# Optimization experiments

Measured on AMD Instinct MI355X. Metric: run time of the kernel, lower is better.

The kernel has to match this reference:

```python
import jax, jax.numpy as jnp
import numpy as np

B, N, NP, NS = 8, 4096, 1024, 32
CF = 64            # input point-feature channels; in_channel = 3 + CF = 67
MLP = [64, 128, 256]
EPS = 1e-5         # BatchNorm eps (torch default)


def setup_inputs() -> dict:
    key = jax.random.key(0)
    ks = jax.random.split(key, 8)
    inp = {
        "xyz": jax.random.normal(ks[0], (B, N, 3), jnp.float32),
        "points": jax.random.normal(ks[1], (B, CF, N), jnp.float32),
        "sample_idx": jax.random.randint(ks[2], (B, NP), 0, N, dtype=jnp.int32),
        "neighbor_idx": jax.random.randint(ks[3], (B, NP, NS), 0, N, dtype=jnp.int32),
    }
    c = 3 + CF
    for i, o in enumerate(MLP):
        wk = jax.random.fold_in(ks[4], i)
        inp[f"W{i}"] = jax.random.normal(wk, (o, c), jnp.float32) * (1.0 / np.sqrt(c))
        inp[f"b{i}"] = jnp.zeros((o,), jnp.float32)
        inp[f"gamma{i}"] = jnp.ones((o,), jnp.float32)
        inp[f"beta{i}"] = jnp.zeros((o,), jnp.float32)
        c = o
    return inp


def _forward(xyz, points, sample_idx, neighbor_idx, params):
    # xyz: (B,N,3)  points: (B,CF,N)
    new_xyz = jnp.take_along_axis(xyz, sample_idx[:, :, None], axis=1)        # (B,NP,3)
    nbr_xyz = jax.vmap(lambda x, idx: x[idx])(xyz, neighbor_idx)               # (B,NP,NS,3)
    rel = nbr_xyz - new_xyz[:, :, None, :]                                     # (B,NP,NS,3)
    nbr_feat = jax.vmap(lambda f, idx: f[:, idx])(points, neighbor_idx)        # (B,CF,NP,NS)
    x = jnp.concatenate([rel.transpose(0, 3, 1, 2), nbr_feat], axis=1)         # (B,3+CF,NP,NS)
    # 1x1 Conv2d -> BatchNorm2d (training-mode batch stats) -> ReLU stack
    for W, b, g, be in params:
        x = jnp.einsum('oc,bcps->bops', W, x) + b[None, :, None, None]
        mu = x.mean(axis=(0, 2, 3), keepdims=True)
        var = x.var(axis=(0, 2, 3), keepdims=True)
        x = g[None, :, None, None] * (x - mu) * jax.lax.rsqrt(var + EPS) + be[None, :, None, None]
        x = jax.nn.relu(x)
    new_points = x.max(axis=-1)                                                # (B,C_out,NP)
    return new_xyz, new_points


def reference(xyz, points, sample_idx, neighbor_idx,
              W0, b0, gamma0, beta0,
              W1, b1, gamma1, beta1,
              W2, b2, gamma2, beta2):
    params = [(W0, b0, gamma0, beta0), (W1, b1, gamma1, beta1), (W2, b2, gamma2, beta2)]
    return _forward(xyz, points, sample_idx, neighbor_idx, params)
```

## Files before the change

### kernel.cpp

```cpp
#include <hip/hip_runtime.h>

typedef unsigned short u16;
typedef unsigned int u32;
typedef __attribute__((ext_vector_type(8))) short short8;
typedef __attribute__((ext_vector_type(16))) float f32x16;

#define BB 8
#define NN 4096
#define NPP 1024
#define NSS 32
#define CFF 64
#define C0 67
#define H0 64
#define H1 128
#define H2 256
#define NTOT (BB*NN)
#define MTOT (BB*NPP*NSS)
#define BN_EPS 1e-5f
#define INV_M (1.0f/262144.0f)
#define NSLOT 64
#define SQOFF 16384
#define LSTRIDE 32768

#define MFMA32(a,b,c) __builtin_amdgcn_mfma_f32_32x32x16_bf16(a,b,c,0,0,0)

__device__ __forceinline__ float bf2f(u16 h){ return __uint_as_float(((u32)h)<<16); }
__device__ __forceinline__ u16 f2bf(float f){
  u32 u = __float_as_uint(f);
  u32 r = (u + 0x7fffu + ((u>>16)&1u)) >> 16;
  return (u16)r;
}
__device__ __forceinline__ u32 pack2(float a, float b){
  return (u32)f2bf(a) | ((u32)f2bf(b)<<16);
}

#define WS_NEED 42434560u

__global__ __launch_bounds__(256) void k_setup(
    const float* __restrict__ xyz, const int* __restrict__ sidx,
    const float* __restrict__ W0, const float* __restrict__ W1, const float* __restrict__ W2,
    u16* __restrict__ Wt0c, u16* __restrict__ Wt1c, u16* __restrict__ Wt2c,
    float* __restrict__ out_newxyz)
{
  int blk = blockIdx.x, tid = threadIdx.x;
  if (blk < 32) {
    int t0 = blk*256 + tid;
    int b = t0 >> 10;
    int s = sidx[t0];
    for (int k = 0; k < 3; ++k)
      out_newxyz[(size_t)t0*3 + k] = xyz[((size_t)(b*NN + s))*3 + k];
  } else if (blk == 32) {
    for (int i = 0; i < 20; ++i) {
      int e = i*256 + tid;
      if (e >= 5120) break;
      int kc = e >> 9, o = (e >> 3) & 63, j = e & 7;
      float v;
      if (kc < 8)       v = W0[o*C0 + 3 + kc*8 + j];
      else if (kc == 8) v = (j < 3) ? W0[o*C0 + j] : 0.f;
      else              v = 0.f;
      Wt0c[e] = f2bf(v);
    }
  } else if (blk == 33) {
    for (int i = 0; i < 32; ++i) {
      int e = i*256 + tid;
      int kc = e >> 10, n = (e >> 3) & 127, j = e & 7;
      Wt1c[e] = f2bf(W1[n*H0 + kc*8 + j]);
    }
  } else {
    int base = (blk - 34) * 4096;
    for (int i = 0; i < 16; ++i) {
      int e = base + i*256 + tid;
      int kc = e >> 11, n = (e >> 3) & 255, j = e & 7;
      Wt2c[e] = f2bf(W2[n*H1 + kc*8 + j]);
    }
  }
}

__global__ __launch_bounds__(256) void k_xyz_only(
    const float* __restrict__ xyz, const int* __restrict__ sidx, float* __restrict__ out_newxyz)
{
  int t0 = blockIdx.x*256 + threadIdx.x;
  int b = t0 >> 10;
  int s = sidx[t0];
  for (int k = 0; k < 3; ++k)
    out_newxyz[(size_t)t0*3 + k] = xyz[((size_t)(b*NN + s))*3 + k];
}

__global__ __launch_bounds__(256) void k_fin(
    const float* __restrict__ stIn, const float* __restrict__ gma,
    const float* __restrict__ bta, int nch,
    float* __restrict__ sclG, float* __restrict__ sftG)
{
  int c = threadIdx.x;
  if (c < nch) {
    float s = 0.f, q = 0.f;
    for (int sl = 0; sl < NSLOT; ++sl) { s += stIn[sl*256 + c]; q += stIn[SQOFF + sl*256 + c]; }
    float mu = s*INV_M, var = q*INV_M - mu*mu;
    float sc = gma[c] * rsqrtf(var + BN_EPS);
    sclG[c] = sc; sftG[c] = bta[c] - mu*sc;
  }
}

__global__ __launch_bounds__(256) void k_uv(
    const float* __restrict__ xyz, const float* __restrict__ points,
    const u16* __restrict__ Wt0c, u16* __restrict__ U, u16* __restrict__ T)
{
  __shared__ u16 XLc[10*128*8];
  __shared__ u16 W0c[10*64*8];
  int tid = threadIdx.x;
  int gn0 = blockIdx.x * 128;
  int b = gn0 >> 12;
  int n0 = gn0 & 4095;

  for (int i = 0; i < 3; ++i) {
    int e = i*256 + tid;
    if (e < 640) ((uint4*)W0c)[e] = ((const uint4*)Wt0c)[e];
  }
  {
    int c = tid >> 2, nseg = tid & 3;
    const float* src = points + ((size_t)(b*CFF + c))*NN + n0 + nseg*32;
    int cb = c >> 3, cr = c & 7;
    for (int t = 0; t < 8; ++t) {
      float4 v = *(const float4*)(src + t*4);
      int n = nseg*32 + t*4;
      XLc[(cb*128 + n+0)*8 + cr] = f2bf(v.x);
      XLc[(cb*128 + n+1)*8 + cr] = f2bf(v.y);
      XLc[(cb*128 + n+2)*8 + cr] = f2bf(v.z);
      XLc[(cb*128 + n+3)*8 + cr] = f2bf(v.w);
    }
  }
  if (tid < 128) {
    int gn = gn0 + tid;
    float x = xyz[(size_t)gn*3+0], y = xyz[(size_t)gn*3+1], z = xyz[(size_t)gn*3+2];
    uint4 v = { pack2(x,y), pack2(z,0.f), 0u, 0u };
    *(uint4*)&XLc[(8*128 + tid)*8] = v;
  } else {
    uint4 z4 = {0u,0u,0u,0u};
    *(uint4*)&XLc[(9*128 + (tid-128))*8] = z4;
  }
  __syncthreads();

  int lane = tid & 63, wv = tid >> 6, l31 = lane & 31, kh = lane >> 5;
  int nt = wv & 1, mtb = (wv >> 1)*2;
  f32x16 accT2[2], accU2[2];
  for (int mi = 0; mi < 2; ++mi) for (int r = 0; r < 16; ++r) accT2[mi][r] = 0.f;

  {
    int ck = 8 + kh;
    short8 bfrag = *(const short8*)&W0c[(ck*64 + nt*32 + l31)*8];
    for (int mi = 0; mi < 2; ++mi) {
      short8 afrag = *(const short8*)&XLc[(ck*128 + (mtb+mi)*32 + l31)*8];
      accT2[mi] = MFMA32(afrag, bfrag, accT2[mi]);
    }
  }
  for (int mi = 0; mi < 2; ++mi) accU2[mi] = accT2[mi];
  for (int kt = 0; kt < 4; ++kt) {
    int ck = kt*2 + kh;
    short8 bfrag = *(const short8*)&W0c[(ck*64 + nt*32 + l31)*8];
    for (int mi = 0; mi < 2; ++mi) {
      short8 afrag = *(const short8*)&XLc[(ck*128 + (mtb+mi)*32 + l31)*8];
      accU2[mi] = MFMA32(afrag, bfrag, accU2[mi]);
    }
  }

  int c = nt*32 + l31;
  for (int mi = 0; mi < 2; ++mi)
    for (int r = 0; r < 16; ++r) {
      int gm = gn0 + (mtb+mi)*32 + (r&3) + 8*(r>>2) + 4*kh;
      U[(size_t)gm*64 + c] = f2bf(accU2[mi][r]);
      T[(size_t)gm*64 + c] = f2bf(accT2[mi][r]);
    }
}

__global__ __launch_bounds__(256) void k_s0y(
    const int* __restrict__ sidx, const int* __restrict__ nidx,
    const u16* __restrict__ U, const u16* __restrict__ T,
    u16* __restrict__ y0, float* __restrict__ stats)
{
  int tid = threadIdx.x;
  int m0 = blockIdx.x * 128;
  int b = m0 >> 15;
  int c0 = (tid & 7) * 8;
  int rg = tid >> 3;
  int wv = tid >> 6;
  int mbase = m0 + rg*4;
  int p = (mbase & 32767) >> 5;
  int sp = sidx[b*NPP + p];
  u16 tv[8];
  *(uint4*)tv = *(const uint4*)(T + ((size_t)(b*NN + sp))*64 + c0);
  float tf[8], s[8], q[8];
  for (int j = 0; j < 8; ++j) { tf[j] = bf2f(tv[j]); s[j] = 0.f; q[j] = 0.f; }
  int nb[4];
  for (int i = 0; i < 4; ++i) nb[i] = nidx[mbase + i];
  for (int i = 0; i < 4; ++i) {
    u16 uv[8], ov[8];
    *(uint4*)uv = *(const uint4*)(U + ((size_t)(b*NN + nb[i]))*64 + c0);
    for (int j = 0; j < 8; ++j) {
      float d = bf2f(uv[j]) - tf[j];
      s[j] += d; q[j] += d*d;
      ov[j] = f2bf(d);
    }
    *(uint4*)(y0 + ((size_t)(mbase + i))*64 + c0) = *(uint4*)ov;
  }
  for (int msk = 8; msk <= 32; msk <<= 1)
    for (int j = 0; j < 8; ++j) {
      s[j] += __shfl_xor(s[j], msk);
      q[j] += __shfl_xor(q[j], msk);
    }
  if ((tid & 63) < 8) {
    int slot = (blockIdx.x*4 + wv) & 63;
    for (int j = 0; j < 8; ++j) {
      atomicAdd(&stats[slot*256 + c0 + j], s[j]);
      atomicAdd(&stats[SQOFF + slot*256 + c0 + j], q[j]);
    }
  }
}

__global__ __launch_bounds__(256) void k_l1s(
    const u16* __restrict__ y0, const u16* __restrict__ Wt1c,
    const float* __restrict__ sclG0, const float* __restrict__ sftG0,
    float* __restrict__ stOut)
{
  __shared__ u16 X0c[8*128*8];
  __shared__ u16 W1c[8*128*8];
  __shared__ float scl0[64], sft0[64];
  int tid = threadIdx.x;
  int m0 = blockIdx.x * 128;

  if (tid < 64) { scl0[tid] = sclG0[tid]; sft0[tid] = sftG0[tid]; }
  for (int i = 0; i < 4; ++i)
    ((uint4*)W1c)[i*256 + tid] = ((const uint4*)Wt1c)[i*256 + tid];

  int pos = tid & 127, half = tid >> 7;
  {
    const u16* row = y0 + (size_t)(m0 + pos)*64 + half*32;
    u16 hs[32];
    for (int t = 0; t < 4; ++t) *(uint4*)&hs[t*8] = ((const uint4*)row)[t];
    __syncthreads();
    u16 ob[32];
    for (int j = 0; j < 32; ++j) {
      int c = half*32 + j;
      ob[j] = f2bf(fmaxf(fmaf(scl0[c], bf2f(hs[j]), sft0[c]), 0.f));
    }
    for (int t = 0; t < 4; ++t)
      *(uint4*)&X0c[((half*4+t)*128 + pos)*8] = *(uint4*)&ob[t*8];
  }
  __syncthreads();

  int lane = tid & 63, wv = tid >> 6, l31 = lane & 31, kh = lane >> 5;
  f32x16 acc[4];
  for (int mt = 0; mt < 4; ++mt) for (int r = 0; r < 16; ++r) acc[mt][r] = 0.f;

  for (int kt = 0; kt < 4; ++kt) {
    int ck = kt*2 + kh;
    short8 bfrag = *(const short8*)&W1c[(ck*128 + wv*32 + l31)*8];
    for (int mt = 0; mt < 4; ++mt) {
      short8 afrag = *(const short8*)&X0c[(ck*128 + mt*32 + l31)*8];
      acc[mt] = MFMA32(afrag, bfrag, acc[mt]);
    }
  }

  float s = 0.f, q = 0.f;
  for (int mt = 0; mt < 4; ++mt)
    for (int r = 0; r < 16; ++r) { float y = acc[mt][r]; s += y; q += y*y; }
  s += __shfl_xor(s, 32); q += __shfl_xor(q, 32);
  if (lane < 32) {
    int slot = (blockIdx.x*4 + wv) & 63;
    atomicAdd(&stOut[slot*256 + wv*32 + lane], s);
    atomicAdd(&stOut[SQOFF + slot*256 + wv*32 + lane], q);
  }
}

__global__ __launch_bounds__(256) void k_l2f(
    const u16* __restrict__ y0,
    const u16* __restrict__ Wt1c, const u16* __restrict__ Wt2c,
    const float* __restrict__ sclG0, const float* __restrict__ sftG0,
    const float* __restrict__ sclG1, const float* __restrict__ sftG1,
    float* __restrict__ stOut, u16* __restrict__ mxp, u16* __restrict__ mnp)
{
  __shared__ u16 X1c[16*520];
  __shared__ u16 UB[16384];
  __shared__ float scl0[64], sft0[64], scl1[128], sft1[128];
  int tid = threadIdx.x;
  int m0 = blockIdx.x * 64;

  if (tid < 64) { scl0[tid] = sclG0[tid]; sft0[tid] = sftG0[tid]; }
  if (tid < 128) { scl1[tid] = sclG1[tid]; sft1[tid] = sftG1[tid]; }
  u16* X0c = UB;
  u16* W1c = UB + 4096;
  for (int i = 0; i < 4; ++i)
    ((uint4*)W1c)[i*256 + tid] = ((const uint4*)Wt1c)[i*256 + tid];

  int pos = tid & 63, grp = tid >> 6;
  {
    const u16* row = y0 + (size_t)(m0 + pos)*64 + grp*16;
    u16 hs[16];
    *(uint4*)&hs[0] = ((const uint4*)row)[0];
    *(uint4*)&hs[8] = ((const uint4*)row)[1];
    __syncthreads();
    u16 ob[16];
    for (int j = 0; j < 16; ++j) {
      int c = grp*16 + j;
      ob[j] = f2bf(fmaxf(fmaf(scl0[c], bf2f(hs[j]), sft0[c]), 0.f));
    }
    *(uint4*)&X0c[((2*grp)*64 + pos)*8]   = *(uint4*)&ob[0];
    *(uint4*)&X0c[((2*grp+1)*64 + pos)*8] = *(uint4*)&ob[8];
  }
  __syncthreads();

  int lane = tid & 63, wv = tid >> 6, l31 = lane & 31, kh = lane >> 5;

  f32x16 acc1[2];
  for (int nt = 0; nt < 2; ++nt) for (int r = 0; r < 16; ++r) acc1[nt][r] = 0.f;
  for (int kt = 0; kt < 4; ++kt) {
    int ck = kt*2 + kh;
    short8 afrag = *(const short8*)&W1c[(ck*128 + wv*32 + l31)*8];
    for (int nt = 0; nt < 2; ++nt) {
      short8 bfrag = *(const short8*)&X0c[(ck*64 + nt*32 + l31)*8];
      acc1[nt] = MFMA32(afrag, bfrag, acc1[nt]);
    }
  }
  __syncthreads();

  {
    float s1r[16], f1r[16];
    for (int r = 0; r < 16; ++r) {
      int ch = wv*32 + (r&3) + 8*(r>>2) + 4*kh;
      s1r[r] = scl1[ch]; f1r[r] = sft1[ch];
    }
    for (int nt = 0; nt < 2; ++nt) {
      int posn = nt*32 + l31;
      for (int g = 0; g < 4; ++g) {
        float v0 = fmaxf(fmaf(s1r[g*4+0], acc1[nt][g*4+0], f1r[g*4+0]), 0.f);
        float v1 = fmaxf(fmaf(s1r[g*4+1], acc1[nt][g*4+1], f1r[g*4+1]), 0.f);
        float v2 = fmaxf(fmaf(s1r[g*4+2], acc1[nt][g*4+2], f1r[g*4+2]), 0.f);
        float v3 = fmaxf(fmaf(s1r[g*4+3], acc1[nt][g*4+3], f1r[g*4+3]), 0.f);
        uint2 w = { pack2(v0, v1), pack2(v2, v3) };
        *(uint2*)&X1c[(wv*4 + g)*520 + posn*8 + 4*kh] = w;
      }
    }
  }
  __syncthreads();

  f32x16 acc2[2][2];
  for (int nt = 0; nt < 2; ++nt) for (int mt = 0; mt < 2; ++mt)
    for (int r = 0; r < 16; ++r) acc2[nt][mt][r] = 0.f;

  for (int h = 0; h < 2; ++h) {
    for (int i = 0; i < 8; ++i)
      ((uint4*)UB)[i*256 + tid] = ((const uint4*)Wt2c)[h*2048 + i*256 + tid];
    __syncthreads();
    for (int k4 = 0; k4 < 4; ++k4) {
      int ckx = (h*4 + k4)*2 + kh;
      int ckw = k4*2 + kh;
      short8 a[2], bf_[2];
      for (int mt = 0; mt < 2; ++mt) a[mt]  = *(const short8*)&X1c[ckx*520 + (mt*32 + l31)*8];
      for (int nt = 0; nt < 2; ++nt) bf_[nt] = *(const short8*)&UB[(ckw*256 + wv*64 + nt*32 + l31)*8];
      for (int nt = 0; nt < 2; ++nt)
        for (int mt = 0; mt < 2; ++mt)
          acc2[nt][mt] = MFMA32(a[mt], bf_[nt], acc2[nt][mt]);
    }
    __syncthreads();
  }

  int slot = (blockIdx.x*4 + wv) & 63;
  for (int nt = 0; nt < 2; ++nt) {
    float s = 0.f, q = 0.f;
    float mx[2] = {-3.0e38f, -3.0e38f}, mn[2] = {3.0e38f, 3.0e38f};
    for (int mt = 0; mt < 2; ++mt)
      for (int r = 0; r < 16; ++r) {
        float y = acc2[nt][mt][r];
        s += y; q += y*y;
        mx[mt] = fmaxf(mx[mt], y); mn[mt] = fminf(mn[mt], y);
      }
    s += __shfl_xor(s, 32); q += __shfl_xor(q, 32);
    mx[0] = fmaxf(mx[0], __shfl_xor(mx[0], 32));
    mx[1] = fmaxf(mx[1], __shfl_xor(mx[1], 32));
    mn[0] = fminf(mn[0], __shfl_xor(mn[0], 32));
    mn[1] = fminf(mn[1], __shfl_xor(mn[1], 32));
    if (lane < 32) {
      int c = wv*64 + nt*32 + lane;
      atomicAdd(&stOut[slot*256 + c], s);
      atomicAdd(&stOut[SQOFF + slot*256 + c], q);
      for (int mt = 0; mt < 2; ++mt) {
        size_t pr = (size_t)blockIdx.x*2 + mt;
        mxp[pr*H2 + c] = f2bf(mx[mt]);
        mnp[pr*H2 + c] = f2bf(mn[mt]);
      }
    }
  }
}

__global__ __launch_bounds__(256) void k_final(
    const u16* __restrict__ mxp, const u16* __restrict__ mnp,
    const float* __restrict__ sclG2, const float* __restrict__ sftG2,
    float* __restrict__ out_np)
{
  __shared__ float tmp[256][33];
  int tid = threadIdx.x;
  int b = blockIdx.x >> 5;
  int p0 = (blockIdx.x & 31) * 32;

  float sc = sclG2[tid];
  float sh = sftG2[tid];

  for (int pp = 0; pp < 32; ++pp) {
    size_t base = ((size_t)(b*NPP + p0 + pp))*H2 + tid;
    float xv = bf2f(mxp[base]), nv = bf2f(mnp[base]);
    float v = (sc >= 0.f) ? fmaf(sc, xv, sh) : fmaf(sc, nv, sh);
    tmp[tid][pp] = fmaxf(v, 0.f);
  }
  __syncthreads();

  int pl = tid & 31, cg = tid >> 5;
  for (int cc = 0; cc < 32; ++cc) {
    int c = cc*8 + cg;
    out_np[((size_t)b*H2 + c)*NPP + p0 + pl] = tmp[c][pl];
  }
}

extern "C" void kernel_launch(void* const* d_in, const int* in_sizes, int n_in,
                              void* d_out, int out_size, void* d_ws, size_t ws_size,
                              hipStream_t stream)
{
  const float* xyz    = (const float*)d_in[0];
  const float* points = (const float*)d_in[1];
  const int*   sidx   = (const int*)d_in[2];
  const int*   nidx   = (const int*)d_in[3];
  const float* W0 = (const float*)d_in[4];
  const float* g0 = (const float*)d_in[6];
  const float* e0 = (const float*)d_in[7];
  const float* W1 = (const float*)d_in[8];
  const float* g1 = (const float*)d_in[10];
  const float* e1 = (const float*)d_in[11];
  const float* W2 = (const float*)d_in[12];
  const float* g2 = (const float*)d_in[14];
  const float* e2 = (const float*)d_in[15];

  float* out_xyz = (float*)d_out;
  float* out_np  = out_xyz + (size_t)BB*NPP*3;

  if (ws_size < (size_t)WS_NEED) {
    hipMemsetAsync(out_np, 0, (size_t)BB*H2*NPP*4, stream);
    k_xyz_only<<<32, 256, 0, stream>>>(xyz, sidx, out_xyz);
    return;
  }

  char* ws = (char*)d_ws;
  float* stats = (float*)(ws + 0);
  u16*   Wt0c  = (u16*)(ws + 393216);
  u16*   Wt1c  = (u16*)(ws + 403456);
  u16*   Wt2c  = (u16*)(ws + 419840);
  float* bnc   = (float*)(ws + 485376);
  u16*   Ubuf  = (u16*)(ws + 491520);
  u16*   Tbuf  = (u16*)(ws + 4685824);
  u16*   y0    = (u16*)(ws + 8880128);
  u16*   mxp   = Ubuf;
  u16*   mnp   = Tbuf;
  float *scl0G = bnc,        *sft0G = bnc + 256;
  float *scl1G = bnc + 512,  *sft1G = bnc + 768;
  float *scl2G = bnc + 1024, *sft2G = bnc + 1280;

  hipMemsetAsync(stats, 0, 3*LSTRIDE*sizeof(float), stream);
  k_setup<<<42, 256, 0, stream>>>(xyz, sidx, W0, W1, W2, Wt0c, Wt1c, Wt2c, out_xyz);
  k_uv<<<NTOT/128, 256, 0, stream>>>(xyz, points, Wt0c, Ubuf, Tbuf);
  k_s0y<<<MTOT/128, 256, 0, stream>>>(sidx, nidx, Ubuf, Tbuf, y0, stats);
  k_fin<<<1, 256, 0, stream>>>(stats, g0, e0, 64, scl0G, sft0G);
  k_l1s<<<MTOT/128, 256, 0, stream>>>(y0, Wt1c, scl0G, sft0G, stats + LSTRIDE);
  k_fin<<<1, 256, 0, stream>>>(stats + LSTRIDE, g1, e1, 128, scl1G, sft1G);
  k_l2f<<<MTOT/64, 256, 0, stream>>>(y0, Wt1c, Wt2c,
                                     scl0G, sft0G, scl1G, sft1G,
                                     stats + 2*LSTRIDE, mxp, mnp);
  k_fin<<<1, 256, 0, stream>>>(stats + 2*LSTRIDE, g2, e2, 256, scl2G, sft2G);
  k_final<<<256, 256, 0, stream>>>(mxp, mnp, scl2G, sft2G, out_np);
}
```

Before: 207.6 us.

## Fold BN finalize into producer kernels via last-block counters and merge setup into k_uv

Removes the three single-block k_fin launches. Each statistics-producing kernel now bumps a global counter, and the last block to finish reduces the slot partials into scale and shift. The weight-prep kernel is merged into the U/T projection kernel, and each projection block converts W0 into shared memory itself. The W2 staging buffer in k_l2f is shrunk and loaded in four smaller chunks, which trades lower LDS use (possibly higher occupancy) for more barriers. Together these cut launch count and inter-kernel gaps, at the cost of a serialized tail reduction in the last block.

```diff
diff --git a/kernel.cpp b/kernel.cpp
--- a/kernel.cpp
+++ b/kernel.cpp
@@ -34,87 +34,66 @@
   return (u32)f2bf(a) | ((u32)f2bf(b)<<16);
 }
 
-#define WS_NEED 42434560u
-
-__global__ __launch_bounds__(256) void k_setup(
-    const float* __restrict__ xyz, const int* __restrict__ sidx,
+#define WS_NEED 42424576u
+
+__global__ __launch_bounds__(256) void k_xyz_only(
+    const float* __restrict__ xyz, const int* __restrict__ sidx, float* __restrict__ out_newxyz)
+{
+  int t0 = blockIdx.x*256 + threadIdx.x;
+  int b = t0 >> 10;
+  int s = sidx[t0];
+  for (int k = 0; k < 3; ++k)
+    out_newxyz[(size_t)t0*3 + k] = xyz[((size_t)(b*NN + s))*3 + k];
+}
+
+__global__ __launch_bounds__(256) void k_init(
+    const float* __restrict__ xyz, const float* __restrict__ points,
+    const int* __restrict__ sidx,
     const float* __restrict__ W0, const float* __restrict__ W1, const float* __restrict__ W2,
-    u16* __restrict__ Wt0c, u16* __restrict__ Wt1c, u16* __restrict__ Wt2c,
-    float* __restrict__ out_newxyz)
+    u16* __restrict__ Wt1c, u16* __restrict__ Wt2c,
+    u16* __restrict__ U, u16* __restrict__ T, float* __restrict__ out_newxyz)
 {
   int blk = blockIdx.x, tid = threadIdx.x;
-  if (blk < 32) {
-    int t0 = blk*256 + tid;
-    int b = t0 >> 10;
-    int s = sidx[t0];
-    for (int k = 0; k < 3; ++k)
-      out_newxyz[(size_t)t0*3 + k] = xyz[((size_t)(b*NN + s))*3 + k];
-  } else if (blk == 32) {
-    for (int i = 0; i < 20; ++i) {
-      int e = i*256 + tid;
-      if (e >= 5120) break;
+  if (blk >= 256) {
+    if (blk < 288) {
+      int t0 = (blk - 256)*256 + tid;
+      int b = t0 >> 10;
+      int s = sidx[t0];
+      for (int k = 0; k < 3; ++k)
+        out_newxyz[(size_t)t0*3 + k] = xyz[((size_t)(b*NN + s))*3 + k];
+    } else if (blk == 288) {
+      for (int i = 0; i < 32; ++i) {
+        int e = i*256 + tid;
+        int kc = e >> 10, n = (e >> 3) & 127, j = e & 7;
+        Wt1c[e] = f2bf(W1[n*H0 + kc*8 + j]);
+      }
+    } else {
+      int base = (blk - 289) * 4096;
+      for (int i = 0; i < 16; ++i) {
+        int e = base + i*256 + tid;
+        int kc = e >> 11, n = (e >> 3) & 255, j = e & 7;
+        Wt2c[e] = f2bf(W2[n*H1 + kc*8 + j]);
+      }
+    }
+    return;
+  }
+
+  __shared__ u16 XLc[10*128*8];
+  __shared__ u16 W0c[10*64*8];
+  int gn0 = blk * 128;
+  int b = gn0 >> 12;
+  int n0 = gn0 & 4095;
+
+  for (int i = 0; i < 20; ++i) {
+    int e = i*256 + tid;
+    if (e < 5120) {
       int kc = e >> 9, o = (e >> 3) & 63, j = e & 7;
       float v;
       if (kc < 8)       v = W0[o*C0 + 3 + kc*8 + j];
       else if (kc == 8) v = (j < 3) ? W0[o*C0 + j] : 0.f;
       else              v = 0.f;
-      Wt0c[e] = f2bf(v);
-    }
-  } else if (blk == 33) {
-    for (int i = 0; i < 32; ++i) {
-      int e = i*256 + tid;
-      int kc = e >> 10, n = (e >> 3) & 127, j = e & 7;
-      Wt1c[e] = f2bf(W1[n*H0 + kc*8 + j]);
-    }
-  } else {
-    int base = (blk - 34) * 4096;
-    for (int i = 0; i < 16; ++i) {
-      int e = base + i*256 + tid;
-      int kc = e >> 11, n = (e >> 3) & 255, j = e & 7;
-      Wt2c[e] = f2bf(W2[n*H1 + kc*8 + j]);
-    }
-  }
-}
-
-__global__ __launch_bounds__(256) void k_xyz_only(
-    const float* __restrict__ xyz, const int* __restrict__ sidx, float* __restrict__ out_newxyz)
-{
-  int t0 = blockIdx.x*256 + threadIdx.x;
-  int b = t0 >> 10;
-  int s = sidx[t0];
-  for (int k = 0; k < 3; ++k)
-    out_newxyz[(size_t)t0*3 + k] = xyz[((size_t)(b*NN + s))*3 + k];
-}
-
-__global__ __launch_bounds__(256) void k_fin(
-    const float* __restrict__ stIn, const float* __restrict__ gma,
-    const float* __restrict__ bta, int nch,
-    float* __restrict__ sclG, float* __restrict__ sftG)
-{
-  int c = threadIdx.x;
-  if (c < nch) {
-    float s = 0.f, q = 0.f;
-    for (int sl = 0; sl < NSLOT; ++sl) { s += stIn[sl*256 + c]; q += stIn[SQOFF + sl*256 + c]; }
-    float mu = s*INV_M, var = q*INV_M - mu*mu;
-    float sc = gma[c] * rsqrtf(var + BN_EPS);
-    sclG[c] = sc; sftG[c] = bta[c] - mu*sc;
-  }
-}
-
-__global__ __launch_bounds__(256) void k_uv(
-    const float* __restrict__ xyz, const float* __restrict__ points,
-    const u16* __restrict__ Wt0c, u16* __restrict__ U, u16* __restrict__ T)
-{
-  __shared__ u16 XLc[10*128*8];
-  __shared__ u16 W0c[10*64*8];
-  int tid = threadIdx.x;
-  int gn0 = blockIdx.x * 128;
-  int b = gn0 >> 12;
-  int n0 = gn0 & 4095;
-
-  for (int i = 0; i < 3; ++i) {
-    int e = i*256 + tid;
-    if (e < 640) ((uint4*)W0c)[e] = ((const uint4*)Wt0c)[e];
+      W0c[e] = f2bf(v);
+    }
   }
   {
     int c = tid >> 2, nseg = tid & 3;
@@ -175,8 +154,11 @@
 __global__ __launch_bounds__(256) void k_s0y(
     const int* __restrict__ sidx, const int* __restrict__ nidx,
     const u16* __restrict__ U, const u16* __restrict__ T,
-    u16* __restrict__ y0, float* __restrict__ stats)
-{
+    u16* __restrict__ y0, float* __restrict__ stats, u32* __restrict__ cnt,
+    const float* __restrict__ gma, const float* __restrict__ bta,
+    float* __restrict__ sclG, float* __restrict__ sftG)
+{
+  __shared__ int isLast;
   int tid = threadIdx.x;
   int m0 = blockIdx.x * 128;
   int b = m0 >> 15;
@@ -214,16 +196,36 @@
       atomicAdd(&stats[SQOFF + slot*256 + c0 + j], q[j]);
     }
   }
+  __syncthreads();
+  if (tid == 0) {
+    __threadfence();
+    u32 old = atomicAdd(cnt, 1u);
+    isLast = (old == gridDim.x - 1);
+  }
+  __syncthreads();
+  if (isLast && tid < H0) {
+    float ss = 0.f, qq = 0.f;
+    for (int sl = 0; sl < NSLOT; ++sl) {
+      ss += atomicAdd(&stats[sl*256 + tid], 0.f);
+      qq += atomicAdd(&stats[SQOFF + sl*256 + tid], 0.f);
+    }
+    float mu = ss*INV_M, var = qq*INV_M - mu*mu;
+    float sc = gma[tid] * rsqrtf(var + BN_EPS);
+    sclG[tid] = sc; sftG[tid] = bta[tid] - mu*sc;
+  }
 }
 
 __global__ __launch_bounds__(256) void k_l1s(
     const u16* __restrict__ y0, const u16* __restrict__ Wt1c,
     const float* __restrict__ sclG0, const float* __restrict__ sftG0,
-    float* __restrict__ stOut)
+    float* __restrict__ stOut, u32* __restrict__ cnt,
+    const float* __restrict__ gma, const float* __restrict__ bta,
+    float* __restrict__ sclG, float* __restrict__ sftG)
 {
   __shared__ u16 X0c[8*128*8];
   __shared__ u16 W1c[8*128*8];
   __shared__ float scl0[64], sft0[64];
+  __shared__ int isLast;
   int tid = threadIdx.x;
   int m0 = blockIdx.x * 128;
 
@@ -269,6 +271,23 @@
     atomicAdd(&stOut[slot*256 + wv*32 + lane], s);
     atomicAdd(&stOut[SQOFF + slot*256 + wv*32 + lane], q);
   }
+  __syncthreads();
+  if (tid == 0) {
+    __threadfence();
+    u32 old = atomicAdd(cnt, 1u);
+    isLast = (old == gridDim.x - 1);
+  }
+  __syncthreads();
+  if (isLast && tid < H1) {
+    float ss = 0.f, qq = 0.f;
+    for (int sl = 0; sl < NSLOT; ++sl) {
+      ss += atomicAdd(&stOut[sl*256 + tid], 0.f);
+      qq += atomicAdd(&stOut[SQOFF + sl*256 + tid], 0.f);
+    }
+    float mu = ss*INV_M, var = qq*INV_M - mu*mu;
+    float sc = gma[tid] * rsqrtf(var + BN_EPS);
+    sclG[tid] = sc; sftG[tid] = bta[tid] - mu*sc;
+  }
 }
 
 __global__ __launch_bounds__(256) void k_l2f(
@@ -276,18 +295,22 @@
     const u16* __restrict__ Wt1c, const u16* __restrict__ Wt2c,
     const float* __restrict__ sclG0, const float* __restrict__ sftG0,
     const float* __restrict__ sclG1, const float* __restrict__ sftG1,
-    float* __restrict__ stOut, u16* __restrict__ mxp, u16* __restrict__ mnp)
+    float* __restrict__ stOut, u16* __restrict__ mxp, u16* __restrict__ mnp,
+    u32* __restrict__ cnt,
+    const float* __restrict__ gma, const float* __restrict__ bta,
+    float* __restrict__ sclG, float* __restrict__ sftG)
 {
   __shared__ u16 X1c[16*520];
-  __shared__ u16 UB[16384];
+  __shared__ u16 A[12288];
   __shared__ float scl0[64], sft0[64], scl1[128], sft1[128];
+  __shared__ int isLast;
   int tid = threadIdx.x;
   int m0 = blockIdx.x * 64;
 
   if (tid < 64) { scl0[tid] = sclG0[tid]; sft0[tid] = sftG0[tid]; }
   if (tid < 128) { scl1[tid] = sclG1[tid]; sft1[tid] = sftG1[tid]; }
-  u16* X0c = UB;
-  u16* W1c = UB + 4096;
+  u16* X0c = A;
+  u16* W1c = A + 4096;
   for (int i = 0; i < 4; ++i)
     ((uint4*)W1c)[i*256 + tid] = ((const uint4*)Wt1c)[i*256 + tid];
 
@@ -340,27 +363,26 @@
       }
     }
   }
-  __syncthreads();
 
   f32x16 acc2[2][2];
   for (int nt = 0; nt < 2; ++nt) for (int mt = 0; mt < 2; ++mt)
     for (int r = 0; r < 16; ++r) acc2[nt][mt][r] = 0.f;
 
-  for (int h = 0; h < 2; ++h) {
-    for (int i = 0; i < 8; ++i)
-      ((uint4*)UB)[i*256 + tid] = ((const uint4*)Wt2c)[h*2048 + i*256 + tid];
+  for (int h = 0; h < 4; ++h) {
     __syncthreads();
-    for (int k4 = 0; k4 < 4; ++k4) {
-      int ckx = (h*4 + k4)*2 + kh;
+    for (int i = 0; i < 4; ++i)
+      ((uint4*)A)[i*256 + tid] = ((const uint4*)Wt2c)[h*1024 + i*256 + tid];
+    __syncthreads();
+    for (int k4 = 0; k4 < 2; ++k4) {
       int ckw = k4*2 + kh;
+      int ckx = h*4 + ckw;
       short8 a[2], bf_[2];
       for (int mt = 0; mt < 2; ++mt) a[mt]  = *(const short8*)&X1c[ckx*520 + (mt*32 + l31)*8];
-      for (int nt = 0; nt < 2; ++nt) bf_[nt] = *(const short8*)&UB[(ckw*256 + wv*64 + nt*32 + l31)*8];
+      for (int nt = 0; nt < 2; ++nt) bf_[nt] = *(const short8*)&A[(ckw*256 + wv*64 + nt*32 + l31)*8];
       for (int nt = 0; nt < 2; ++nt)
         for (int mt = 0; mt < 2; ++mt)
           acc2[nt][mt] = MFMA32(a[mt], bf_[nt], acc2[nt][mt]);
     }
-    __syncthreads();
   }
 
   int slot = (blockIdx.x*4 + wv) & 63;
@@ -389,6 +411,23 @@
       }
     }
   }
+  __syncthreads();
+  if (tid == 0) {
+    __threadfence();
+    u32 old = atomicAdd(cnt, 1u);
+    isLast = (old == gridDim.x - 1);
+  }
+  __syncthreads();
+  if (isLast) {
+    float ss = 0.f, qq = 0.f;
+    for (int sl = 0; sl < NSLOT; ++sl) {
+      ss += atomicAdd(&stOut[sl*256 + tid], 0.f);
+      qq += atomicAdd(&stOut[SQOFF + sl*256 + tid], 0.f);
+    }
+    float mu = ss*INV_M, var = qq*INV_M - mu*mu;
+    float sc = gma[tid] * rsqrtf(var + BN_EPS);
+    sclG[tid] = sc; sftG[tid] = bta[tid] - mu*sc;
+  }
 }
 
 __global__ __launch_bounds__(256) void k_final(
@@ -447,30 +486,30 @@
   }
 
   char* ws = (char*)d_ws;
-  float* stats = (float*)(ws + 0);
-  u16*   Wt0c  = (u16*)(ws + 393216);
-  u16*   Wt1c  = (u16*)(ws + 403456);
-  u16*   Wt2c  = (u16*)(ws + 419840);
-  float* bnc   = (float*)(ws + 485376);
-  u16*   Ubuf  = (u16*)(ws + 491520);
-  u16*   Tbuf  = (u16*)(ws + 4685824);
-  u16*   y0    = (u16*)(ws + 8880128);
+  u32*   cnt   = (u32*)(ws + 0);
+  float* stats = (float*)(ws + 256);
+  u16*   Wt1c  = (u16*)(ws + 393472);
+  u16*   Wt2c  = (u16*)(ws + 409856);
+  float* bnc   = (float*)(ws + 475392);
+  u16*   Ubuf  = (u16*)(ws + 481536);
+  u16*   Tbuf  = (u16*)(ws + 4675840);
+  u16*   y0    = (u16*)(ws + 8870144);
   u16*   mxp   = Ubuf;
   u16*   mnp   = Tbuf;
   float *scl0G = bnc,        *sft0G = bnc + 256;
   float *scl1G = bnc + 512,  *sft1G = bnc + 768;
   float *scl2G = bnc + 1024, *sft2G = bnc + 1280;
 
-  hipMemsetAsync(stats, 0, 3*LSTRIDE*sizeof(float), stream);
-  k_setup<<<42, 256, 0, stream>>>(xyz, sidx, W0, W1, W2, Wt0c, Wt1c, Wt2c, out_xyz);
-  k_uv<<<NTOT/128, 256, 0, stream>>>(xyz, points, Wt0c, Ubuf, Tbuf);
-  k_s0y<<<MTOT/128, 256, 0, stream>>>(sidx, nidx, Ubuf, Tbuf, y0, stats);
-  k_fin<<<1, 256, 0, stream>>>(stats, g0, e0, 64, scl0G, sft0G);
-  k_l1s<<<MTOT/128, 256, 0, stream>>>(y0, Wt1c, scl0G, sft0G, stats + LSTRIDE);
-  k_fin<<<1, 256, 0, stream>>>(stats + LSTRIDE, g1, e1, 128, scl1G, sft1G);
+  hipMemsetAsync(ws, 0, 393472, stream);
+  k_init<<<297, 256, 0, stream>>>(xyz, points, sidx, W0, W1, W2,
+                                  Wt1c, Wt2c, Ubuf, Tbuf, out_xyz);
+  k_s0y<<<MTOT/128, 256, 0, stream>>>(sidx, nidx, Ubuf, Tbuf, y0,
+                                      stats, cnt + 0, g0, e0, scl0G, sft0G);
+  k_l1s<<<MTOT/128, 256, 0, stream>>>(y0, Wt1c, scl0G, sft0G,
+                                      stats + LSTRIDE, cnt + 1, g1, e1, scl1G, sft1G);
   k_l2f<<<MTOT/64, 256, 0, stream>>>(y0, Wt1c, Wt2c,
                                      scl0G, sft0G, scl1G, sft1G,
-                                     stats + 2*LSTRIDE, mxp, mnp);
-  k_fin<<<1, 256, 0, stream>>>(stats + 2*LSTRIDE, g2, e2, 256, scl2G, sft2G);
+                                     stats + 2*LSTRIDE, mxp, mnp,
+                                     cnt + 2, g2, e2, scl2G, sft2G);
   k_final<<<256, 256, 0, stream>>>(mxp, mnp, scl2G, sft2G, out_np);
 }
```

Measured after the change: 405.4 us. 95.3% more time.
